# Kernel optimization log

Measured on AMD Instinct MI355X. Metric: run time of the kernel, lower is better.

Reference implementation:

```python
import jax, jax.numpy as jnp
import numpy as np

D_IN = 128
D_OUT = 128
B, N = 8, 2048
NEG = -9e15


def setup_inputs() -> dict:
    key = jax.random.key(0)
    ks = jax.random.split(key, 7)
    x = jax.random.normal(ks[0], (B, N, D_IN), dtype=jnp.float32)
    adj = jax.random.randint(ks[1], (B, N, N), 0, 2).astype(jnp.float32)
    s_in = 1.0 / np.sqrt(D_IN)
    s_out = 1.0 / np.sqrt(D_OUT)
    s_g = 1.0 / np.sqrt(2 * D_OUT)
    # torch.nn.Linear weights stored pre-transposed: [in, out]
    W_w = jax.random.uniform(ks[2], (D_IN, D_OUT), jnp.float32, -s_in, s_in)
    W_b = jax.random.uniform(ks[3], (D_OUT,), jnp.float32, -s_in, s_in)
    A_w = jax.random.uniform(ks[4], (D_OUT, D_OUT), jnp.float32, -s_out, s_out)
    gate_w = jax.random.uniform(ks[5], (2 * D_OUT, 1), jnp.float32, -s_g, s_g)
    gate_b = jax.random.uniform(ks[6], (1,), jnp.float32, -s_g, s_g)
    return {"x": x, "adj": adj, "W_w": W_w, "W_b": W_b, "A_w": A_w,
            "gate_w": gate_w, "gate_b": gate_b}


def reference(x, adj, W_w, W_b, A_w, gate_w, gate_b):
    h = x @ W_w + W_b                                  # [B,N,D]
    e = jnp.einsum('bnd,bmd->bnm', h @ A_w, h)          # [B,N,N]
    e = e + jnp.swapaxes(e, 1, 2)                       # symmetric
    att = jnp.where(adj > 0, e, NEG)
    att = jax.nn.softmax(att, axis=1)                   # NOTE: dim=1 as in torch code
    att = att * adj
    h_prime = jax.nn.relu(jnp.einsum('bnm,bmd->bnd', att, h))
    coeff = jax.nn.sigmoid(jnp.concatenate([x, h_prime], axis=-1) @ gate_w + gate_b)  # [B,N,1]
    return coeff * x + (1.0 - coeff) * h_prime
```

## Files before the change

### kernel.cpp

```cpp
#include <hip/hip_runtime.h>
#include <hip/hip_bf16.h>

#define B_ 8
#define N_ 2048
#define D_ 128

typedef __bf16 bf16_t;
typedef __bf16 v8bf __attribute__((ext_vector_type(8)));
typedef float  v4f  __attribute__((ext_vector_type(4)));

__global__ __launch_bounds__(256) void k_prep(
    const float* __restrict__ Ww, const float* __restrict__ Aw,
    bf16_t* __restrict__ WT, bf16_t* __restrict__ AT)
{
    int idx = blockIdx.x * 256 + threadIdx.x;
    int o = idx >> 7, i = idx & 127;
    WT[idx] = (bf16_t)Ww[i * D_ + o];
    AT[idx] = (bf16_t)Aw[i * D_ + o];
}

__global__ __launch_bounds__(256) void k_mask(
    const float* __restrict__ adj, unsigned int* __restrict__ mk)
{
    int w = blockIdx.x * 256 + threadIdx.x;
    const float* src = adj + (size_t)w * 32;
    unsigned int bits = 0;
#pragma unroll
    for (int k = 0; k < 8; ++k) {
        float4 f = *(const float4*)(src + k * 4);
        bits |= (f.x > 0.f ? 1u : 0u) << (k * 4 + 0);
        bits |= (f.y > 0.f ? 1u : 0u) << (k * 4 + 1);
        bits |= (f.z > 0.f ? 1u : 0u) << (k * 4 + 2);
        bits |= (f.w > 0.f ? 1u : 0u) << (k * 4 + 3);
    }
    mk[w] = bits;
}

__global__ __launch_bounds__(256) void k_hg(
    const float* __restrict__ x, const float* __restrict__ Wb,
    const bf16_t* __restrict__ WT, const bf16_t* __restrict__ AT,
    bf16_t* __restrict__ hb, bf16_t* __restrict__ gb)
{
    int wave = threadIdx.x >> 6;
    int lane = threadIdx.x & 63;
    int q = lane >> 4;
    int c = lane & 15;
    int nrow0 = blockIdx.x * 64 + wave * 16;

    __shared__ float pw_all[4][16][132];
    float (*pw)[132] = pw_all[wave];

    v8bf ax[4];
#pragma unroll
    for (int kc = 0; kc < 4; ++kc) {
        const float* src = x + (size_t)(nrow0 + c) * D_ + kc * 32 + q * 8;
        float4 f0 = *(const float4*)src;
        float4 f1 = *(const float4*)(src + 4);
        v8bf a;
        a[0]=(bf16_t)f0.x; a[1]=(bf16_t)f0.y; a[2]=(bf16_t)f0.z; a[3]=(bf16_t)f0.w;
        a[4]=(bf16_t)f1.x; a[5]=(bf16_t)f1.y; a[6]=(bf16_t)f1.z; a[7]=(bf16_t)f1.w;
        ax[kc] = a;
    }

#pragma unroll
    for (int ct = 0; ct < 8; ++ct) {
        float bias = Wb[ct * 16 + c];
        v4f acc = {bias, bias, bias, bias};
#pragma unroll
        for (int kc = 0; kc < 4; ++kc) {
            v8bf bw = *(const v8bf*)(WT + (size_t)(ct * 16 + c) * D_ + kc * 32 + q * 8);
            acc = __builtin_amdgcn_mfma_f32_16x16x32_bf16(ax[kc], bw, acc, 0, 0, 0);
        }
#pragma unroll
        for (int r = 0; r < 4; ++r) pw[q * 4 + r][ct * 16 + c] = acc[r];
    }
    __builtin_amdgcn_wave_barrier();

    v8bf ahf[4];
#pragma unroll
    for (int kc = 0; kc < 4; ++kc) {
        v4f p0 = *(const v4f*)&pw[c][kc * 32 + q * 8];
        v4f p1 = *(const v4f*)&pw[c][kc * 32 + q * 8 + 4];
        v8bf a;
#pragma unroll
        for (int j = 0; j < 4; ++j) { a[j] = (bf16_t)p0[j]; a[j+4] = (bf16_t)p1[j]; }
        ahf[kc] = a;
    }
    {
        int row = lane >> 2, seg = lane & 3;
#pragma unroll
        for (int v = 0; v < 4; ++v) {
            v8bf hv;
#pragma unroll
            for (int j = 0; j < 8; ++j) hv[j] = (bf16_t)pw[row][seg * 32 + v * 8 + j];
            *(v8bf*)(hb + (size_t)(nrow0 + row) * D_ + seg * 32 + v * 8) = hv;
        }
    }
    __builtin_amdgcn_wave_barrier();

#pragma unroll
    for (int ct = 0; ct < 8; ++ct) {
        v4f acc = {0.f, 0.f, 0.f, 0.f};
#pragma unroll
        for (int kc = 0; kc < 4; ++kc) {
            v8bf bw = *(const v8bf*)(AT + (size_t)(ct * 16 + c) * D_ + kc * 32 + q * 8);
            acc = __builtin_amdgcn_mfma_f32_16x16x32_bf16(ahf[kc], bw, acc, 0, 0, 0);
        }
#pragma unroll
        for (int r = 0; r < 4; ++r) pw[q * 4 + r][ct * 16 + c] = acc[r];
    }
    __builtin_amdgcn_wave_barrier();
    {
        int row = lane >> 2, seg = lane & 3;
#pragma unroll
        for (int v = 0; v < 4; ++v) {
            v8bf gv;
#pragma unroll
            for (int j = 0; j < 8; ++j) gv[j] = (bf16_t)pw[row][seg * 32 + v * 8 + j];
            *(v8bf*)(gb + (size_t)(nrow0 + row) * D_ + seg * 32 + v * 8) = gv;
        }
    }
}

__global__ __launch_bounds__(256, 2) void k_att(
    const bf16_t* __restrict__ hb, const bf16_t* __restrict__ gb,
    const unsigned int* __restrict__ mk, float* __restrict__ colsum,
    bf16_t* __restrict__ Pt)
{
    int bid = blockIdx.x;
    int b = bid & 7;
    int rest = bid >> 3;
    int nblk = rest >> 3;
    int mgrp = rest & 7;
    int wave = threadIdx.x >> 6;
    int lane = threadIdx.x & 63;
    int q = lane >> 4;
    int c = lane & 15;
    int nbase = nblk * 64;
    int mwav = mgrp * 256 + wave * 64;
    const size_t hgoff = (size_t)b * N_ * D_;
    const unsigned int* mkb = mk + (size_t)b * N_ * (N_ / 32);

    __shared__ bf16_t eb_all[4][64][72];
    bf16_t (*eb)[72] = eb_all[wave];

    uint2 wq[4][4];
#pragma unroll
    for (int sub = 0; sub < 4; ++sub)
#pragma unroll
        for (int r = 0; r < 4; ++r) {
            int row = nbase + sub * 16 + q * 4 + r;
            wq[sub][r] = *(const uint2*)(mkb + (size_t)row * (N_ / 32) + (mwav >> 5));
        }

    v8bf ag[4][4], ah[4][4];
#pragma unroll
    for (int sub = 0; sub < 4; ++sub)
#pragma unroll
        for (int kc = 0; kc < 4; ++kc) {
            size_t off = hgoff + (size_t)(nbase + sub * 16 + c) * D_ + kc * 32 + q * 8;
            ag[sub][kc] = *(const v8bf*)(gb + off);
            ah[sub][kc] = *(const v8bf*)(hb + off);
        }

#pragma unroll
    for (int t = 0; t < 4; ++t) {
        int mt = mwav + t * 16;
        v8bf bh[4], bg[4];
#pragma unroll
        for (int kc = 0; kc < 4; ++kc) {
            size_t off = hgoff + (size_t)(mt + c) * D_ + kc * 32 + q * 8;
            bh[kc] = *(const v8bf*)(hb + off);
            bg[kc] = *(const v8bf*)(gb + off);
        }
        v4f e[4];
#pragma unroll
        for (int sub = 0; sub < 4; ++sub) e[sub] = (v4f){0.f, 0.f, 0.f, 0.f};
#pragma unroll
        for (int kc = 0; kc < 4; ++kc)
#pragma unroll
            for (int sub = 0; sub < 4; ++sub) {
                e[sub] = __builtin_amdgcn_mfma_f32_16x16x32_bf16(ag[sub][kc], bh[kc], e[sub], 0, 0, 0);
                e[sub] = __builtin_amdgcn_mfma_f32_16x16x32_bf16(ah[sub][kc], bg[kc], e[sub], 0, 0, 0);
            }
        unsigned int sh = (unsigned)((t & 1) * 16 + c);
        float cs = 0.f;
#pragma unroll
        for (int sub = 0; sub < 4; ++sub)
#pragma unroll
            for (int r = 0; r < 4; ++r) {
                unsigned int wv = (t >> 1) ? wq[sub][r].y : wq[sub][r].x;
                float ex = __expf(e[sub][r]);
                float pv = ((wv >> sh) & 1u) ? ex : 0.f;
                eb[sub * 16 + q * 4 + r][t * 16 + c] = (bf16_t)pv;
                cs += pv;
            }
        cs += __shfl_xor(cs, 16);
        cs += __shfl_xor(cs, 32);
        if (lane < 16) atomicAdd(&colsum[b * N_ + mt + lane], cs);
    }
    __builtin_amdgcn_wave_barrier();
    int prow = lane >> 3, pseg = lane & 7;
#pragma unroll
    for (int pass = 0; pass < 8; ++pass) {
        int row = pass * 8 + prow;
        v8bf o = *(const v8bf*)&eb[row][pseg * 8];
        *(v8bf*)(Pt + ((size_t)b * N_ + nbase + row) * N_ + mwav + pseg * 8) = o;
    }
}

__global__ __launch_bounds__(256) void k_scaleT(
    const bf16_t* __restrict__ hb, const float* __restrict__ colsum,
    bf16_t* __restrict__ hbTs)
{
    int bid = blockIdx.x;
    int b = bid >> 6;
    int rem = bid & 63;
    int nblk = rem >> 1;
    int dblk = rem & 1;
    int tid = threadIdx.x;
    __shared__ bf16_t sm[64][72];
    __shared__ float sinv[64];
    int n0 = nblk * 64, d0 = dblk * 64;
    int r = tid >> 3, cg = tid & 7;
#pragma unroll
    for (int rr = 0; rr < 2; ++rr) {
        int row = r + rr * 32;
        *(v8bf*)&sm[row][cg * 8] =
            *(const v8bf*)(hb + (size_t)(b * N_ + n0 + row) * D_ + d0 + cg * 8);
    }
    if (tid < 64) {
        float s = colsum[b * N_ + n0 + tid];
        sinv[tid] = (s > 0.f) ? 1.f / s : 0.f;
    }
    __syncthreads();
#pragma unroll
    for (int rr = 0; rr < 2; ++rr) {
        int dr = r + rr * 32;
        v8bf v;
#pragma unroll
        for (int jj = 0; jj < 8; ++jj)
            v[jj] = (bf16_t)((float)sm[cg * 8 + jj][dr] * sinv[cg * 8 + jj]);
        *(v8bf*)(hbTs + (size_t)(b * D_ + d0 + dr) * N_ + n0 + cg * 8) = v;
    }
}

__global__ __launch_bounds__(512, 2) void k_out(
    const bf16_t* __restrict__ Pt, const bf16_t* __restrict__ hbTs,
    const float* __restrict__ x, const float* __restrict__ gw,
    const float* __restrict__ gbias, float* __restrict__ out)
{
    int bid = blockIdx.x;
    int b = bid & 7;
    int nblk = bid >> 3;
    int tid = threadIdx.x;
    int wave = tid >> 6;
    int lane = tid & 63;
    int q = lane >> 4;
    int c = lane & 15;
    int nbase = nblk * 64;
    int m0 = wave * 256;

    __shared__ float hp[64][132];

    const bf16_t* hTb = hbTs + (size_t)b * D_ * N_;
    const bf16_t* Pb  = Pt + (size_t)b * N_ * N_;

    v4f acc[4][8];
#pragma unroll
    for (int sub = 0; sub < 4; ++sub)
#pragma unroll
        for (int dt = 0; dt < 8; ++dt) acc[sub][dt] = (v4f){0.f, 0.f, 0.f, 0.f};

    for (int ch = 0; ch < 8; ++ch) {
        int mch = m0 + ch * 32;
        v8bf a[4];
#pragma unroll
        for (int sub = 0; sub < 4; ++sub)
            a[sub] = *(const v8bf*)(Pb + (size_t)(nbase + sub * 16 + c) * N_ + mch + q * 8);
        v8bf vt[8];
#pragma unroll
        for (int dt = 0; dt < 8; ++dt)
            vt[dt] = *(const v8bf*)(hTb + (size_t)(dt * 16 + c) * N_ + mch + q * 8);
#pragma unroll
        for (int dt = 0; dt < 8; ++dt)
#pragma unroll
            for (int sub = 0; sub < 4; ++sub)
                acc[sub][dt] = __builtin_amdgcn_mfma_f32_16x16x32_bf16(a[sub], vt[dt], acc[sub][dt], 0, 0, 0);
    }

    if (wave == 0) {
#pragma unroll
        for (int sub = 0; sub < 4; ++sub)
#pragma unroll
            for (int dt = 0; dt < 8; ++dt)
#pragma unroll
                for (int r = 0; r < 4; ++r)
                    hp[sub * 16 + q * 4 + r][dt * 16 + c] = acc[sub][dt][r];
    }
    __syncthreads();
#pragma unroll
    for (int wv = 1; wv < 8; ++wv) {
        if (wave == wv) {
#pragma unroll
            for (int sub = 0; sub < 4; ++sub)
#pragma unroll
                for (int dt = 0; dt < 8; ++dt)
#pragma unroll
                    for (int r = 0; r < 4; ++r)
                        hp[sub * 16 + q * 4 + r][dt * 16 + c] += acc[sub][dt][r];
        }
        __syncthreads();
    }

    int row = tid >> 3;
    int seg = tid & 7;
    size_t g = (size_t)b * N_ + nbase + row;
    const float* xr = x + g * D_ + seg * 16;
    float xv[16], hv[16];
#pragma unroll
    for (int j = 0; j < 16; j += 4) {
        float4 f = *(const float4*)(xr + j);
        xv[j] = f.x; xv[j+1] = f.y; xv[j+2] = f.z; xv[j+3] = f.w;
    }
#pragma unroll
    for (int j = 0; j < 16; ++j) hv[j] = fmaxf(hp[row][seg * 16 + j], 0.f);
    float part = 0.f;
#pragma unroll
    for (int j = 0; j < 16; ++j)
        part += xv[j] * gw[seg * 16 + j] + hv[j] * gw[D_ + seg * 16 + j];
    part += __shfl_xor(part, 1);
    part += __shfl_xor(part, 2);
    part += __shfl_xor(part, 4);
    float coeff = 1.f / (1.f + __expf(-(part + gbias[0])));
    float* orow = out + g * D_ + seg * 16;
#pragma unroll
    for (int j = 0; j < 16; j += 4) {
        float4 o;
        o.x = coeff * xv[j]   + (1.f - coeff) * hv[j];
        o.y = coeff * xv[j+1] + (1.f - coeff) * hv[j+1];
        o.z = coeff * xv[j+2] + (1.f - coeff) * hv[j+2];
        o.w = coeff * xv[j+3] + (1.f - coeff) * hv[j+3];
        *(float4*)(orow + j) = o;
    }
}

extern "C" void kernel_launch(void* const* d_in, const int* in_sizes, int n_in,
                              void* d_out, int out_size, void* d_ws, size_t ws_size,
                              hipStream_t stream)
{
    const float* x     = (const float*)d_in[0];
    const float* adj   = (const float*)d_in[1];
    const float* Ww    = (const float*)d_in[2];
    const float* Wb    = (const float*)d_in[3];
    const float* Aw    = (const float*)d_in[4];
    const float* gw    = (const float*)d_in[5];
    const float* gbias = (const float*)d_in[6];
    float* out = (float*)d_out;

    char* ws = (char*)d_ws;
    bf16_t* hb     = (bf16_t*)(ws);
    bf16_t* gb     = (bf16_t*)(ws + (4 << 20));
    bf16_t* hbTs   = (bf16_t*)(ws + (8 << 20));
    float*  colsum = (float*)(ws + (12 << 20));
    unsigned int* mkw = (unsigned int*)(ws + (13 << 20));
    bf16_t* Pt     = (bf16_t*)(ws + (17 << 20));
    bf16_t* WT     = (bf16_t*)(ws + (81 << 20));
    bf16_t* AT     = (bf16_t*)(ws + (81 << 20) + (32 << 10));

    hipMemsetAsync(colsum, 0, B_ * N_ * sizeof(float), stream);
    k_prep<<<64, 256, 0, stream>>>(Ww, Aw, WT, AT);
    k_mask<<<B_ * N_ * (N_ / 32) / 256, 256, 0, stream>>>(adj, mkw);
    k_hg<<<B_ * N_ / 64, 256, 0, stream>>>(x, Wb, WT, AT, hb, gb);
    k_att<<<2048, 256, 0, stream>>>(hb, gb, mkw, colsum, Pt);
    k_scaleT<<<512, 256, 0, stream>>>(hb, colsum, hbTs);
    k_out<<<256, 512, 0, stream>>>(Pt, hbTs, x, gw, gbias, out);
}
```

Measured before the change: 334.4 us.

## Recompute attention scores in output kernel instead of materializing P matrix

Stops writing the full B×N×N bf16 attention matrix to global memory. A first pass (k_cs) computes only the masked exp column sums. The output kernel (k_pv) then recomputes the scores with MFMA, applies the mask and exp, stages P in shared memory and multiplies it by the scaled h. This removes 64MB of writes and reads in exchange for doing the score GEMM and exp twice. It also changes block shapes and needs a per-chunk __syncthreads.

```diff
diff --git a/kernel.cpp b/kernel.cpp
--- a/kernel.cpp
+++ b/kernel.cpp
@@ -4,6 +4,7 @@
 #define B_ 8
 #define N_ 2048
 #define D_ 128
+#define NW_ (N_ / 32)
 
 typedef __bf16 bf16_t;
 typedef __bf16 v8bf __attribute__((ext_vector_type(8)));
@@ -122,90 +123,63 @@
     }
 }
 
-__global__ __launch_bounds__(256, 2) void k_att(
+__global__ __launch_bounds__(256) void k_cs(
     const bf16_t* __restrict__ hb, const bf16_t* __restrict__ gb,
-    const unsigned int* __restrict__ mk, float* __restrict__ colsum,
-    bf16_t* __restrict__ Pt)
+    const unsigned int* __restrict__ mk, float* __restrict__ colsum)
 {
     int bid = blockIdx.x;
     int b = bid & 7;
-    int rest = bid >> 3;
-    int nblk = rest >> 3;
-    int mgrp = rest & 7;
+    int mblk = bid >> 3;
     int wave = threadIdx.x >> 6;
     int lane = threadIdx.x & 63;
-    int q = lane >> 4;
-    int c = lane & 15;
-    int nbase = nblk * 64;
-    int mwav = mgrp * 256 + wave * 64;
+    int q = lane >> 4, c = lane & 15;
+    int m0 = mblk * 32;
     const size_t hgoff = (size_t)b * N_ * D_;
-    const unsigned int* mkb = mk + (size_t)b * N_ * (N_ / 32);
-
-    __shared__ bf16_t eb_all[4][64][72];
-    bf16_t (*eb)[72] = eb_all[wave];
-
-    uint2 wq[4][4];
-#pragma unroll
-    for (int sub = 0; sub < 4; ++sub)
+    const unsigned int* mkb = mk + (size_t)b * N_ * NW_;
+
+    v8bf bh[2][4], bg2[2][4];
+#pragma unroll
+    for (int ms = 0; ms < 2; ++ms)
+#pragma unroll
+        for (int kc = 0; kc < 4; ++kc) {
+            size_t off = hgoff + (size_t)(m0 + ms * 16 + c) * D_ + kc * 32 + q * 8;
+            bh[ms][kc]  = *(const v8bf*)(hb + off);
+            bg2[ms][kc] = *(const v8bf*)(gb + off);
+        }
+
+    float cs0 = 0.f, cs1 = 0.f;
+    for (int j = 0; j < 32; ++j) {
+        int n0 = j * 64 + wave * 16;
+        v8bf ah[4], ag[4];
+#pragma unroll
+        for (int kc = 0; kc < 4; ++kc) {
+            size_t off = hgoff + (size_t)(n0 + c) * D_ + kc * 32 + q * 8;
+            ah[kc] = *(const v8bf*)(hb + off);
+            ag[kc] = *(const v8bf*)(gb + off);
+        }
+        unsigned int mw[4];
+#pragma unroll
+        for (int r = 0; r < 4; ++r)
+            mw[r] = mkb[(size_t)(n0 + q * 4 + r) * NW_ + mblk];
+        v4f e0 = {0.f,0.f,0.f,0.f}, e1 = {0.f,0.f,0.f,0.f};
+#pragma unroll
+        for (int kc = 0; kc < 4; ++kc) {
+            e0 = __builtin_amdgcn_mfma_f32_16x16x32_bf16(ag[kc], bh[0][kc], e0, 0, 0, 0);
+            e0 = __builtin_amdgcn_mfma_f32_16x16x32_bf16(ah[kc], bg2[0][kc], e0, 0, 0, 0);
+            e1 = __builtin_amdgcn_mfma_f32_16x16x32_bf16(ag[kc], bh[1][kc], e1, 0, 0, 0);
+            e1 = __builtin_amdgcn_mfma_f32_16x16x32_bf16(ah[kc], bg2[1][kc], e1, 0, 0, 0);
+        }
 #pragma unroll
         for (int r = 0; r < 4; ++r) {
-            int row = nbase + sub * 16 + q * 4 + r;
-            wq[sub][r] = *(const uint2*)(mkb + (size_t)row * (N_ / 32) + (mwav >> 5));
-        }
-
-    v8bf ag[4][4], ah[4][4];
-#pragma unroll
-    for (int sub = 0; sub < 4; ++sub)
-#pragma unroll
-        for (int kc = 0; kc < 4; ++kc) {
-            size_t off = hgoff + (size_t)(nbase + sub * 16 + c) * D_ + kc * 32 + q * 8;
-            ag[sub][kc] = *(const v8bf*)(gb + off);
-            ah[sub][kc] = *(const v8bf*)(hb + off);
-        }
-
-#pragma unroll
-    for (int t = 0; t < 4; ++t) {
-        int mt = mwav + t * 16;
-        v8bf bh[4], bg[4];
-#pragma unroll
-        for (int kc = 0; kc < 4; ++kc) {
-            size_t off = hgoff + (size_t)(mt + c) * D_ + kc * 32 + q * 8;
-            bh[kc] = *(const v8bf*)(hb + off);
-            bg[kc] = *(const v8bf*)(gb + off);
-        }
-        v4f e[4];
-#pragma unroll
-        for (int sub = 0; sub < 4; ++sub) e[sub] = (v4f){0.f, 0.f, 0.f, 0.f};
-#pragma unroll
-        for (int kc = 0; kc < 4; ++kc)
-#pragma unroll
-            for (int sub = 0; sub < 4; ++sub) {
-                e[sub] = __builtin_amdgcn_mfma_f32_16x16x32_bf16(ag[sub][kc], bh[kc], e[sub], 0, 0, 0);
-                e[sub] = __builtin_amdgcn_mfma_f32_16x16x32_bf16(ah[sub][kc], bg[kc], e[sub], 0, 0, 0);
-            }
-        unsigned int sh = (unsigned)((t & 1) * 16 + c);
-        float cs = 0.f;
-#pragma unroll
-        for (int sub = 0; sub < 4; ++sub)
-#pragma unroll
-            for (int r = 0; r < 4; ++r) {
-                unsigned int wv = (t >> 1) ? wq[sub][r].y : wq[sub][r].x;
-                float ex = __expf(e[sub][r]);
-                float pv = ((wv >> sh) & 1u) ? ex : 0.f;
-                eb[sub * 16 + q * 4 + r][t * 16 + c] = (bf16_t)pv;
-                cs += pv;
-            }
-        cs += __shfl_xor(cs, 16);
-        cs += __shfl_xor(cs, 32);
-        if (lane < 16) atomicAdd(&colsum[b * N_ + mt + lane], cs);
-    }
-    __builtin_amdgcn_wave_barrier();
-    int prow = lane >> 3, pseg = lane & 7;
-#pragma unroll
-    for (int pass = 0; pass < 8; ++pass) {
-        int row = pass * 8 + prow;
-        v8bf o = *(const v8bf*)&eb[row][pseg * 8];
-        *(v8bf*)(Pt + ((size_t)b * N_ + nbase + row) * N_ + mwav + pseg * 8) = o;
+            cs0 += ((mw[r] >> c) & 1u) ? __expf(e0[r]) : 0.f;
+            cs1 += ((mw[r] >> (16 + c)) & 1u) ? __expf(e1[r]) : 0.f;
+        }
+    }
+    cs0 += __shfl_xor(cs0, 16);  cs0 += __shfl_xor(cs0, 32);
+    cs1 += __shfl_xor(cs1, 16);  cs1 += __shfl_xor(cs1, 32);
+    if (lane < 16) {
+        atomicAdd(&colsum[b * N_ + m0 + lane], cs0);
+        atomicAdd(&colsum[b * N_ + m0 + 16 + lane], cs1);
     }
 }
 
@@ -245,8 +219,9 @@
     }
 }
 
-__global__ __launch_bounds__(512, 2) void k_out(
-    const bf16_t* __restrict__ Pt, const bf16_t* __restrict__ hbTs,
+__global__ __launch_bounds__(256) void k_pv(
+    const bf16_t* __restrict__ hb, const bf16_t* __restrict__ gb,
+    const unsigned int* __restrict__ mk, const bf16_t* __restrict__ hbTs,
     const float* __restrict__ x, const float* __restrict__ gw,
     const float* __restrict__ gbias, float* __restrict__ out)
 {
@@ -256,62 +231,85 @@
     int tid = threadIdx.x;
     int wave = tid >> 6;
     int lane = tid & 63;
-    int q = lane >> 4;
-    int c = lane & 15;
-    int nbase = nblk * 64;
-    int m0 = wave * 256;
-
-    __shared__ float hp[64][132];
-
+    int q = lane >> 4, c = lane & 15;
+    int nbase = nblk * 32;
+    int nsub = wave >> 1;
+    int mh = wave & 1;
+
+    __shared__ bf16_t P[2][32][72];
+    __shared__ float hp[32][132];
+
+    const size_t hgoff = (size_t)b * N_ * D_;
+    const unsigned int* mkb = mk + (size_t)b * N_ * NW_;
     const bf16_t* hTb = hbTs + (size_t)b * D_ * N_;
-    const bf16_t* Pb  = Pt + (size_t)b * N_ * N_;
-
-    v4f acc[4][8];
-#pragma unroll
-    for (int sub = 0; sub < 4; ++sub)
-#pragma unroll
-        for (int dt = 0; dt < 8; ++dt) acc[sub][dt] = (v4f){0.f, 0.f, 0.f, 0.f};
-
-    for (int ch = 0; ch < 8; ++ch) {
-        int mch = m0 + ch * 32;
-        v8bf a[4];
-#pragma unroll
-        for (int sub = 0; sub < 4; ++sub)
-            a[sub] = *(const v8bf*)(Pb + (size_t)(nbase + sub * 16 + c) * N_ + mch + q * 8);
-        v8bf vt[8];
-#pragma unroll
-        for (int dt = 0; dt < 8; ++dt)
-            vt[dt] = *(const v8bf*)(hTb + (size_t)(dt * 16 + c) * N_ + mch + q * 8);
-#pragma unroll
-        for (int dt = 0; dt < 8; ++dt)
-#pragma unroll
-            for (int sub = 0; sub < 4; ++sub)
-                acc[sub][dt] = __builtin_amdgcn_mfma_f32_16x16x32_bf16(a[sub], vt[dt], acc[sub][dt], 0, 0, 0);
-    }
-
-    if (wave == 0) {
-#pragma unroll
-        for (int sub = 0; sub < 4; ++sub)
-#pragma unroll
-            for (int dt = 0; dt < 8; ++dt)
-#pragma unroll
-                for (int r = 0; r < 4; ++r)
-                    hp[sub * 16 + q * 4 + r][dt * 16 + c] = acc[sub][dt][r];
-    }
+
+    v8bf pah[4], pag[4];
+#pragma unroll
+    for (int kc = 0; kc < 4; ++kc) {
+        size_t off = hgoff + (size_t)(nbase + nsub * 16 + c) * D_ + kc * 32 + q * 8;
+        pah[kc] = *(const v8bf*)(hb + off);
+        pag[kc] = *(const v8bf*)(gb + off);
+    }
+
+    v4f acc[2][2];
+#pragma unroll
+    for (int ns = 0; ns < 2; ++ns)
+#pragma unroll
+        for (int dt = 0; dt < 2; ++dt) acc[ns][dt] = (v4f){0.f, 0.f, 0.f, 0.f};
+
+    for (int ch = 0; ch < 32; ++ch) {
+        int mc = ch * 64;
+        int cur = ch & 1;
+        v8bf bh[2][4], bg2[2][4];
+#pragma unroll
+        for (int ms = 0; ms < 2; ++ms)
+#pragma unroll
+            for (int kc = 0; kc < 4; ++kc) {
+                size_t off = hgoff + (size_t)(mc + mh * 32 + ms * 16 + c) * D_ + kc * 32 + q * 8;
+                bh[ms][kc]  = *(const v8bf*)(hb + off);
+                bg2[ms][kc] = *(const v8bf*)(gb + off);
+            }
+        unsigned int mw[4];
+#pragma unroll
+        for (int r = 0; r < 4; ++r)
+            mw[r] = mkb[(size_t)(nbase + nsub * 16 + q * 4 + r) * NW_ + (mc >> 5) + mh];
+        v4f e0 = {0.f,0.f,0.f,0.f}, e1 = {0.f,0.f,0.f,0.f};
+#pragma unroll
+        for (int kc = 0; kc < 4; ++kc) {
+            e0 = __builtin_amdgcn_mfma_f32_16x16x32_bf16(pag[kc], bh[0][kc], e0, 0, 0, 0);
+            e0 = __builtin_amdgcn_mfma_f32_16x16x32_bf16(pah[kc], bg2[0][kc], e0, 0, 0, 0);
+            e1 = __builtin_amdgcn_mfma_f32_16x16x32_bf16(pag[kc], bh[1][kc], e1, 0, 0, 0);
+            e1 = __builtin_amdgcn_mfma_f32_16x16x32_bf16(pah[kc], bg2[1][kc], e1, 0, 0, 0);
+        }
+#pragma unroll
+        for (int r = 0; r < 4; ++r) {
+            float p0 = ((mw[r] >> c) & 1u) ? __expf(e0[r]) : 0.f;
+            float p1 = ((mw[r] >> (16 + c)) & 1u) ? __expf(e1[r]) : 0.f;
+            P[cur][nsub * 16 + q * 4 + r][mh * 32 + c]      = (bf16_t)p0;
+            P[cur][nsub * 16 + q * 4 + r][mh * 32 + 16 + c] = (bf16_t)p1;
+        }
+        __syncthreads();
+#pragma unroll
+        for (int k2 = 0; k2 < 2; ++k2) {
+            v8bf pa0 = *(const v8bf*)&P[cur][c][k2 * 32 + q * 8];
+            v8bf pa1 = *(const v8bf*)&P[cur][16 + c][k2 * 32 + q * 8];
+            v8bf vt0 = *(const v8bf*)(hTb + (size_t)(wave * 32 + c) * N_ + mc + k2 * 32 + q * 8);
+            v8bf vt1 = *(const v8bf*)(hTb + (size_t)(wave * 32 + 16 + c) * N_ + mc + k2 * 32 + q * 8);
+            acc[0][0] = __builtin_amdgcn_mfma_f32_16x16x32_bf16(pa0, vt0, acc[0][0], 0, 0, 0);
+            acc[0][1] = __builtin_amdgcn_mfma_f32_16x16x32_bf16(pa0, vt1, acc[0][1], 0, 0, 0);
+            acc[1][0] = __builtin_amdgcn_mfma_f32_16x16x32_bf16(pa1, vt0, acc[1][0], 0, 0, 0);
+            acc[1][1] = __builtin_amdgcn_mfma_f32_16x16x32_bf16(pa1, vt1, acc[1][1], 0, 0, 0);
+        }
+    }
+
+#pragma unroll
+    for (int ns = 0; ns < 2; ++ns)
+#pragma unroll
+        for (int dt = 0; dt < 2; ++dt)
+#pragma unroll
+            for (int r = 0; r < 4; ++r)
+                hp[ns * 16 + q * 4 + r][wave * 32 + dt * 16 + c] = acc[ns][dt][r];
     __syncthreads();
-#pragma unroll
-    for (int wv = 1; wv < 8; ++wv) {
-        if (wave == wv) {
-#pragma unroll
-            for (int sub = 0; sub < 4; ++sub)
-#pragma unroll
-                for (int dt = 0; dt < 8; ++dt)
-#pragma unroll
-                    for (int r = 0; r < 4; ++r)
-                        hp[sub * 16 + q * 4 + r][dt * 16 + c] += acc[sub][dt][r];
-        }
-        __syncthreads();
-    }
 
     int row = tid >> 3;
     int seg = tid & 7;
@@ -364,15 +362,14 @@
     bf16_t* hbTs   = (bf16_t*)(ws + (8 << 20));
     float*  colsum = (float*)(ws + (12 << 20));
     unsigned int* mkw = (unsigned int*)(ws + (13 << 20));
-    bf16_t* Pt     = (bf16_t*)(ws + (17 << 20));
     bf16_t* WT     = (bf16_t*)(ws + (81 << 20));
     bf16_t* AT     = (bf16_t*)(ws + (81 << 20) + (32 << 10));
 
     hipMemsetAsync(colsum, 0, B_ * N_ * sizeof(float), stream);
     k_prep<<<64, 256, 0, stream>>>(Ww, Aw, WT, AT);
-    k_mask<<<B_ * N_ * (N_ / 32) / 256, 256, 0, stream>>>(adj, mkw);
+    k_mask<<<B_ * N_ * NW_ / 256, 256, 0, stream>>>(adj, mkw);
     k_hg<<<B_ * N_ / 64, 256, 0, stream>>>(x, Wb, WT, AT, hb, gb);
-    k_att<<<2048, 256, 0, stream>>>(hb, gb, mkw, colsum, Pt);
+    k_cs<<<512, 256, 0, stream>>>(hb, gb, mkw, colsum);
     k_scaleT<<<512, 256, 0, stream>>>(hb, colsum, hbTs);
-    k_out<<<256, 512, 0, stream>>>(Pt, hbTs, x, gw, gbias, out);
-}
+    k_pv<<<512, 256, 0, stream>>>(hb, gb, mkw, hbTs, x, gw, gbias, out);
+}
```

New measurement: 449.5 us. +34.5%, slower.

## Symmetrize A in weights to halve attention MFMAs; retile output GEMM

Applied to the files above, without the earlier changes.

The symmetric score e+e^T equals h(A+A^T)h^T, so A+A^T is precomputed once in the prep kernel. The attention kernel then issues one MFMA chain per tile instead of two and drops the extra h/g loads. Separately, the output kernel is retiled: each block now covers 32 rows, and each wave computes a 16x32 output tile over the full K range. This removes the serialized cross-wave LDS reduction and doubles the grid. The trade-off is more redundant global reads of P and h^T per block, plus slightly different bf16 rounding from summing A and A^T before the cast.

```diff
diff --git a/kernel.cpp b/kernel.cpp
--- a/kernel.cpp
+++ b/kernel.cpp
@@ -4,6 +4,7 @@
 #define B_ 8
 #define N_ 2048
 #define D_ 128
+#define NW_ (N_ / 32)
 
 typedef __bf16 bf16_t;
 typedef __bf16 v8bf __attribute__((ext_vector_type(8)));
@@ -11,12 +12,12 @@
 
 __global__ __launch_bounds__(256) void k_prep(
     const float* __restrict__ Ww, const float* __restrict__ Aw,
-    bf16_t* __restrict__ WT, bf16_t* __restrict__ AT)
+    bf16_t* __restrict__ WT, bf16_t* __restrict__ ST)
 {
     int idx = blockIdx.x * 256 + threadIdx.x;
     int o = idx >> 7, i = idx & 127;
     WT[idx] = (bf16_t)Ww[i * D_ + o];
-    AT[idx] = (bf16_t)Aw[i * D_ + o];
+    ST[idx] = (bf16_t)(Aw[i * D_ + o] + Aw[o * D_ + i]);
 }
 
 __global__ __launch_bounds__(256) void k_mask(
@@ -38,7 +39,7 @@
 
 __global__ __launch_bounds__(256) void k_hg(
     const float* __restrict__ x, const float* __restrict__ Wb,
-    const bf16_t* __restrict__ WT, const bf16_t* __restrict__ AT,
+    const bf16_t* __restrict__ WT, const bf16_t* __restrict__ ST,
     bf16_t* __restrict__ hb, bf16_t* __restrict__ gb)
 {
     int wave = threadIdx.x >> 6;
@@ -103,7 +104,7 @@
         v4f acc = {0.f, 0.f, 0.f, 0.f};
 #pragma unroll
         for (int kc = 0; kc < 4; ++kc) {
-            v8bf bw = *(const v8bf*)(AT + (size_t)(ct * 16 + c) * D_ + kc * 32 + q * 8);
+            v8bf bw = *(const v8bf*)(ST + (size_t)(ct * 16 + c) * D_ + kc * 32 + q * 8);
             acc = __builtin_amdgcn_mfma_f32_16x16x32_bf16(ahf[kc], bw, acc, 0, 0, 0);
         }
 #pragma unroll
@@ -139,7 +140,7 @@
     int nbase = nblk * 64;
     int mwav = mgrp * 256 + wave * 64;
     const size_t hgoff = (size_t)b * N_ * D_;
-    const unsigned int* mkb = mk + (size_t)b * N_ * (N_ / 32);
+    const unsigned int* mkb = mk + (size_t)b * N_ * NW_;
 
     __shared__ bf16_t eb_all[4][64][72];
     bf16_t (*eb)[72] = eb_all[wave];
@@ -150,39 +151,33 @@
 #pragma unroll
         for (int r = 0; r < 4; ++r) {
             int row = nbase + sub * 16 + q * 4 + r;
-            wq[sub][r] = *(const uint2*)(mkb + (size_t)row * (N_ / 32) + (mwav >> 5));
-        }
-
-    v8bf ag[4][4], ah[4][4];
+            wq[sub][r] = *(const uint2*)(mkb + (size_t)row * NW_ + (mwav >> 5));
+        }
+
+    v8bf ag[4][4];
 #pragma unroll
     for (int sub = 0; sub < 4; ++sub)
 #pragma unroll
-        for (int kc = 0; kc < 4; ++kc) {
-            size_t off = hgoff + (size_t)(nbase + sub * 16 + c) * D_ + kc * 32 + q * 8;
-            ag[sub][kc] = *(const v8bf*)(gb + off);
-            ah[sub][kc] = *(const v8bf*)(hb + off);
-        }
+        for (int kc = 0; kc < 4; ++kc)
+            ag[sub][kc] = *(const v8bf*)(gb + hgoff
+                + (size_t)(nbase + sub * 16 + c) * D_ + kc * 32 + q * 8);
 
 #pragma unroll
     for (int t = 0; t < 4; ++t) {
         int mt = mwav + t * 16;
-        v8bf bh[4], bg[4];
-#pragma unroll
-        for (int kc = 0; kc < 4; ++kc) {
-            size_t off = hgoff + (size_t)(mt + c) * D_ + kc * 32 + q * 8;
-            bh[kc] = *(const v8bf*)(hb + off);
-            bg[kc] = *(const v8bf*)(gb + off);
-        }
+        v8bf bh[4];
+#pragma unroll
+        for (int kc = 0; kc < 4; ++kc)
+            bh[kc] = *(const v8bf*)(hb + hgoff
+                + (size_t)(mt + c) * D_ + kc * 32 + q * 8);
         v4f e[4];
 #pragma unroll
         for (int sub = 0; sub < 4; ++sub) e[sub] = (v4f){0.f, 0.f, 0.f, 0.f};
 #pragma unroll
         for (int kc = 0; kc < 4; ++kc)
 #pragma unroll
-            for (int sub = 0; sub < 4; ++sub) {
+            for (int sub = 0; sub < 4; ++sub)
                 e[sub] = __builtin_amdgcn_mfma_f32_16x16x32_bf16(ag[sub][kc], bh[kc], e[sub], 0, 0, 0);
-                e[sub] = __builtin_amdgcn_mfma_f32_16x16x32_bf16(ah[sub][kc], bg[kc], e[sub], 0, 0, 0);
-            }
         unsigned int sh = (unsigned)((t & 1) * 16 + c);
         float cs = 0.f;
 #pragma unroll
@@ -258,91 +253,71 @@
     int lane = tid & 63;
     int q = lane >> 4;
     int c = lane & 15;
-    int nbase = nblk * 64;
-    int m0 = wave * 256;
-
-    __shared__ float hp[64][132];
-
-    const bf16_t* hTb = hbTs + (size_t)b * D_ * N_;
-    const bf16_t* Pb  = Pt + (size_t)b * N_ * N_;
-
-    v4f acc[4][8];
-#pragma unroll
-    for (int sub = 0; sub < 4; ++sub)
-#pragma unroll
-        for (int dt = 0; dt < 8; ++dt) acc[sub][dt] = (v4f){0.f, 0.f, 0.f, 0.f};
-
-    for (int ch = 0; ch < 8; ++ch) {
-        int mch = m0 + ch * 32;
-        v8bf a[4];
-#pragma unroll
-        for (int sub = 0; sub < 4; ++sub)
-            a[sub] = *(const v8bf*)(Pb + (size_t)(nbase + sub * 16 + c) * N_ + mch + q * 8);
-        v8bf vt[8];
-#pragma unroll
-        for (int dt = 0; dt < 8; ++dt)
-            vt[dt] = *(const v8bf*)(hTb + (size_t)(dt * 16 + c) * N_ + mch + q * 8);
-#pragma unroll
-        for (int dt = 0; dt < 8; ++dt)
-#pragma unroll
-            for (int sub = 0; sub < 4; ++sub)
-                acc[sub][dt] = __builtin_amdgcn_mfma_f32_16x16x32_bf16(a[sub], vt[dt], acc[sub][dt], 0, 0, 0);
-    }
-
-    if (wave == 0) {
-#pragma unroll
-        for (int sub = 0; sub < 4; ++sub)
-#pragma unroll
-            for (int dt = 0; dt < 8; ++dt)
-#pragma unroll
-                for (int r = 0; r < 4; ++r)
-                    hp[sub * 16 + q * 4 + r][dt * 16 + c] = acc[sub][dt][r];
+    int nbase = nblk * 32;
+    int nsub = wave & 1;
+    int dq = wave >> 1;
+
+    __shared__ float hp[2][16][132];
+
+    const bf16_t* hTb  = hbTs + (size_t)b * D_ * N_;
+    const bf16_t* Arow = Pt + (size_t)b * N_ * N_ + (size_t)(nbase + nsub * 16 + c) * N_;
+    const bf16_t* Br0  = hTb + (size_t)(dq * 32 + c) * N_;
+    const bf16_t* Br1  = hTb + (size_t)(dq * 32 + 16 + c) * N_;
+
+    v4f acc0 = {0.f, 0.f, 0.f, 0.f};
+    v4f acc1 = {0.f, 0.f, 0.f, 0.f};
+#pragma unroll 4
+    for (int ch = 0; ch < 64; ++ch) {
+        int mo = ch * 32 + q * 8;
+        v8bf pa = *(const v8bf*)(Arow + mo);
+        v8bf v0 = *(const v8bf*)(Br0 + mo);
+        v8bf v1 = *(const v8bf*)(Br1 + mo);
+        acc0 = __builtin_amdgcn_mfma_f32_16x16x32_bf16(pa, v0, acc0, 0, 0, 0);
+        acc1 = __builtin_amdgcn_mfma_f32_16x16x32_bf16(pa, v1, acc1, 0, 0, 0);
+    }
+
+#pragma unroll
+    for (int r = 0; r < 4; ++r) {
+        hp[nsub][q * 4 + r][dq * 32 + c]      = acc0[r];
+        hp[nsub][q * 4 + r][dq * 32 + 16 + c] = acc1[r];
     }
     __syncthreads();
-#pragma unroll
-    for (int wv = 1; wv < 8; ++wv) {
-        if (wave == wv) {
-#pragma unroll
-            for (int sub = 0; sub < 4; ++sub)
-#pragma unroll
-                for (int dt = 0; dt < 8; ++dt)
-#pragma unroll
-                    for (int r = 0; r < 4; ++r)
-                        hp[sub * 16 + q * 4 + r][dt * 16 + c] += acc[sub][dt][r];
-        }
-        __syncthreads();
-    }
-
-    int row = tid >> 3;
-    int seg = tid & 7;
+
+    int row = tid >> 4;
+    int seg = tid & 15;
     size_t g = (size_t)b * N_ + nbase + row;
-    const float* xr = x + g * D_ + seg * 16;
-    float xv[16], hv[16];
-#pragma unroll
-    for (int j = 0; j < 16; j += 4) {
-        float4 f = *(const float4*)(xr + j);
-        xv[j] = f.x; xv[j+1] = f.y; xv[j+2] = f.z; xv[j+3] = f.w;
-    }
-#pragma unroll
-    for (int j = 0; j < 16; ++j) hv[j] = fmaxf(hp[row][seg * 16 + j], 0.f);
+    const float* xr = x + g * D_ + seg * 8;
+    float xv[8], hv[8];
+    {
+        float4 f0 = *(const float4*)(xr);
+        float4 f1 = *(const float4*)(xr + 4);
+        xv[0]=f0.x; xv[1]=f0.y; xv[2]=f0.z; xv[3]=f0.w;
+        xv[4]=f1.x; xv[5]=f1.y; xv[6]=f1.z; xv[7]=f1.w;
+    }
+    const float* hrow = &hp[row >> 4][row & 15][seg * 8];
+#pragma unroll
+    for (int j = 0; j < 8; ++j) hv[j] = fmaxf(hrow[j], 0.f);
     float part = 0.f;
 #pragma unroll
-    for (int j = 0; j < 16; ++j)
-        part += xv[j] * gw[seg * 16 + j] + hv[j] * gw[D_ + seg * 16 + j];
+    for (int j = 0; j < 8; ++j)
+        part += xv[j] * gw[seg * 8 + j] + hv[j] * gw[D_ + seg * 8 + j];
     part += __shfl_xor(part, 1);
     part += __shfl_xor(part, 2);
     part += __shfl_xor(part, 4);
+    part += __shfl_xor(part, 8);
     float coeff = 1.f / (1.f + __expf(-(part + gbias[0])));
-    float* orow = out + g * D_ + seg * 16;
-#pragma unroll
-    for (int j = 0; j < 16; j += 4) {
-        float4 o;
-        o.x = coeff * xv[j]   + (1.f - coeff) * hv[j];
-        o.y = coeff * xv[j+1] + (1.f - coeff) * hv[j+1];
-        o.z = coeff * xv[j+2] + (1.f - coeff) * hv[j+2];
-        o.w = coeff * xv[j+3] + (1.f - coeff) * hv[j+3];
-        *(float4*)(orow + j) = o;
-    }
+    float* orow = out + g * D_ + seg * 8;
+    float4 o0, o1;
+    o0.x = coeff * xv[0] + (1.f - coeff) * hv[0];
+    o0.y = coeff * xv[1] + (1.f - coeff) * hv[1];
+    o0.z = coeff * xv[2] + (1.f - coeff) * hv[2];
+    o0.w = coeff * xv[3] + (1.f - coeff) * hv[3];
+    o1.x = coeff * xv[4] + (1.f - coeff) * hv[4];
+    o1.y = coeff * xv[5] + (1.f - coeff) * hv[5];
+    o1.z = coeff * xv[6] + (1.f - coeff) * hv[6];
+    o1.w = coeff * xv[7] + (1.f - coeff) * hv[7];
+    *(float4*)(orow)     = o0;
+    *(float4*)(orow + 4) = o1;
 }
 
 extern "C" void kernel_launch(void* const* d_in, const int* in_sizes, int n_in,
@@ -366,13 +341,13 @@
     unsigned int* mkw = (unsigned int*)(ws + (13 << 20));
     bf16_t* Pt     = (bf16_t*)(ws + (17 << 20));
     bf16_t* WT     = (bf16_t*)(ws + (81 << 20));
-    bf16_t* AT     = (bf16_t*)(ws + (81 << 20) + (32 << 10));
+    bf16_t* ST     = (bf16_t*)(ws + (81 << 20) + (32 << 10));
 
     hipMemsetAsync(colsum, 0, B_ * N_ * sizeof(float), stream);
-    k_prep<<<64, 256, 0, stream>>>(Ww, Aw, WT, AT);
-    k_mask<<<B_ * N_ * (N_ / 32) / 256, 256, 0, stream>>>(adj, mkw);
-    k_hg<<<B_ * N_ / 64, 256, 0, stream>>>(x, Wb, WT, AT, hb, gb);
+    k_prep<<<64, 256, 0, stream>>>(Ww, Aw, WT, ST);
+    k_mask<<<B_ * N_ * NW_ / 256, 256, 0, stream>>>(adj, mkw);
+    k_hg<<<B_ * N_ / 64, 256, 0, stream>>>(x, Wb, WT, ST, hb, gb);
     k_att<<<2048, 256, 0, stream>>>(hb, gb, mkw, colsum, Pt);
     k_scaleT<<<512, 256, 0, stream>>>(hb, colsum, hbTs);
-    k_out<<<256, 512, 0, stream>>>(Pt, hbTs, x, gw, gbias, out);
-}
+    k_out<<<512, 512, 0, stream>>>(Pt, hbTs, x, gw, gbias, out);
+}
```

After: 352.9 us. 5.5% more time.
